# Kernel tuning notes

Hardware: AMD Instinct MI355X
Metric: run time of the kernel (lower is better)

Reference implementation:

```python
import jax, jax.numpy as jnp
import numpy as np

B, S, E, H = 4, 2048, 1024, 16
D = E // H  # head_dim = 64


def setup_inputs() -> dict:
    key0 = jax.random.key(0)
    ks = jax.random.split(key0, 11)
    sc = 1.0 / np.sqrt(E)
    return {
        "query": jax.random.normal(ks[0], (B, S, E), jnp.float32),
        "key": jax.random.normal(ks[1], (B, S, E), jnp.float32),
        "value": jax.random.normal(ks[2], (B, S, E), jnp.float32),
        "Wq": jax.random.normal(ks[3], (E, E), jnp.float32) * sc,
        "bq": jax.random.normal(ks[4], (E,), jnp.float32) * sc,
        "Wk": jax.random.normal(ks[5], (E, E), jnp.float32) * sc,
        "bk": jax.random.normal(ks[6], (E,), jnp.float32) * sc,
        "Wv": jax.random.normal(ks[7], (E, E), jnp.float32) * sc,
        "bv": jax.random.normal(ks[8], (E,), jnp.float32) * sc,
        "Wo": jax.random.normal(ks[9], (E, E), jnp.float32) * sc,
        "bo": jax.random.normal(ks[10], (E,), jnp.float32) * sc,
    }


def reference(query, key, value, Wq, bq, Wk, bk, Wv, bv, Wo, bo):
    b, s, e = query.shape
    q = query @ Wq + bq
    k = key @ Wk + bk
    v = value @ Wv + bv
    # [b, s, E] -> [b, H, s, D]
    qh = q.reshape(b, s, H, D).transpose(0, 2, 1, 3)
    kh = k.reshape(b, s, H, D).transpose(0, 2, 1, 3)
    vh = v.reshape(b, s, H, D).transpose(0, 2, 1, 3)
    energy = jnp.einsum('nhql,nhkl->nhqk', qh, kh)  # [b, H, s, s]
    scale = jnp.asarray(1.0 / np.sqrt(D), energy.dtype)
    attention = jax.nn.softmax(energy * scale, axis=-1)
    # NOTE: faithful to the source einsum 'nhqk,nhvl->nhql' (k and v both contracted)
    out = jnp.einsum('nhqk,nhvl->nhql', attention, vh)  # [b, H, s, D]
    out = out.transpose(0, 2, 1, 3).reshape(b, s, e)
    return out @ Wo + bo
```

## Files before the change

kernel.cpp:

```cpp
#include <hip/hip_runtime.h>
#include <hip/hip_bf16.h>

#define B_ 4
#define S_ 2048
#define E_ 1024

#define ES 16
#define SC 4
#define EPS (E_ / ES)
#define SPC (S_ / SC)
#define NPART (ES * SC)

#define RPB 8

__global__ __launch_bounds__(1024) void k_front(const float* __restrict__ value,
                                                const float* __restrict__ Wv,
                                                const float* __restrict__ bo,
                                                float* __restrict__ tpart,
                                                float* __restrict__ o) {
    const int es = blockIdx.x, sc = blockIdx.y, b = blockIdx.z;
    const int t = threadIdx.x;
    __shared__ float4 red[64][16];
    __shared__ float4 red2[4][16];
    __shared__ float vb[EPS];

    {
        const int c4 = t & 15, rg = t >> 4;
        const float* base = value + ((size_t)b * S_ + (size_t)sc * SPC) * E_
                            + es * EPS + c4 * 4;
        float4 acc = make_float4(0.f, 0.f, 0.f, 0.f);
#pragma unroll
        for (int r = 0; r < 8; ++r) {
            float4 v = *reinterpret_cast<const float4*>(base + (size_t)(rg + r * 64) * E_);
            acc.x += v.x; acc.y += v.y; acc.z += v.z; acc.w += v.w;
        }
        red[rg][c4] = acc;
    }
    __syncthreads();
    if (t < 64) {
        const int c = t & 15, q = t >> 4;
        float4 s = make_float4(0.f, 0.f, 0.f, 0.f);
#pragma unroll
        for (int k = 0; k < 16; ++k) {
            float4 v = red[q * 16 + k][c];
            s.x += v.x; s.y += v.y; s.z += v.z; s.w += v.w;
        }
        red2[q][c] = s;
    }
    __syncthreads();
    if (t < 16) {
        float4 s0 = red2[0][t], s1 = red2[1][t], s2 = red2[2][t], s3 = red2[3][t];
        float4 s = make_float4(s0.x + s1.x + s2.x + s3.x,
                               s0.y + s1.y + s2.y + s3.y,
                               s0.z + s1.z + s2.z + s3.z,
                               s0.w + s1.w + s2.w + s3.w);
        reinterpret_cast<float4*>(vb)[t] = s;
    }
    __syncthreads();

    {
        const float* wv = Wv + (size_t)(es * EPS) * E_ + t;
        float a = 0.f;
#pragma unroll 8
        for (int k = 0; k < EPS; ++k)
            a = fmaf(vb[k], wv[(size_t)k * E_], a);
        tpart[((size_t)(es * SC + sc) * B_ + b) * E_ + t] = a;
    }

    if (es == 0 && sc == 0 && t < 256) {
        reinterpret_cast<float4*>(o + (size_t)b * E_)[t] =
            reinterpret_cast<const float4*>(bo)[t];
    }
}

__global__ __launch_bounds__(256) void k_mid(const float* __restrict__ tpart,
                                             const float* __restrict__ bv,
                                             const float* __restrict__ Wo,
                                             float* __restrict__ o) {
    const int jb = blockIdx.x, b = blockIdx.y;
    const int t = threadIdx.x;
    __shared__ float red[16][16];
    __shared__ float tj[16];

    {
        const int jl = t & 15, pg = t >> 4;
        float s = 0.f;
#pragma unroll
        for (int q = 0; q < 4; ++q) {
            const int p = pg + q * 16;
            s += tpart[((size_t)p * B_ + b) * E_ + jb * 16 + jl];
        }
        red[pg][jl] = s;
    }
    __syncthreads();
    if (t < 16) {
        float v = (float)S_ * bv[jb * 16 + t];
#pragma unroll
        for (int g = 0; g < 16; ++g) v += red[g][t];
        tj[t] = v;
    }
    __syncthreads();

    float oacc[4] = {0.f, 0.f, 0.f, 0.f};
#pragma unroll
    for (int jj = 0; jj < 16; ++jj) {
        const float* wo = Wo + (size_t)(jb * 16 + jj) * E_;
        const float tv = tj[jj];
#pragma unroll
        for (int k2 = 0; k2 < 4; ++k2)
            oacc[k2] = fmaf(tv, wo[k2 * 256 + t], oacc[k2]);
    }
#pragma unroll
    for (int k2 = 0; k2 < 4; ++k2)
        atomicAdd(&o[(size_t)b * E_ + k2 * 256 + t], oacc[k2]);
}

__global__ __launch_bounds__(256) void k_bcast(const float* __restrict__ o,
                                               float* __restrict__ out) {
    const int sb = blockIdx.x, b = blockIdx.y;
    const int t = threadIdx.x;
    float4 ov = reinterpret_cast<const float4*>(o + (size_t)b * E_)[t];
    float4* dst = reinterpret_cast<float4*>(
        out + ((size_t)b * S_ + (size_t)sb * RPB) * E_);
#pragma unroll
    for (int r = 0; r < RPB; ++r)
        dst[r * (E_ / 4) + t] = ov;
}

extern "C" void kernel_launch(void* const* d_in, const int* in_sizes, int n_in,
                              void* d_out, int out_size, void* d_ws, size_t ws_size,
                              hipStream_t stream) {
    const float* value = (const float*)d_in[2];
    const float* Wv    = (const float*)d_in[7];
    const float* bv    = (const float*)d_in[8];
    const float* Wo    = (const float*)d_in[9];
    const float* bo    = (const float*)d_in[10];
    float* out = (float*)d_out;

    float* tpart = (float*)d_ws;
    float* o     = tpart + (size_t)NPART * B_ * E_;

    k_front<<<dim3(ES, SC, B_),    1024, 0, stream>>>(value, Wv, bo, tpart, o);
    k_mid  <<<dim3(NPART, B_),     256,  0, stream>>>(tpart, bv, Wo, o);
    k_bcast<<<dim3(S_ / RPB, B_),  256,  0, stream>>>(o, out);
}
```

Measured before the change: 26.64 us.

## Fuse Wo GEMV and broadcast into a single back kernel, drop atomics

```diff
diff --git a/kernel.cpp b/kernel.cpp
--- a/kernel.cpp
+++ b/kernel.cpp
@@ -11,13 +11,14 @@
 #define SPC (S_ / SC)
 #define NPART (ES * SC)
 
-#define RPB 8
+#define ISL 8
+#define ICW 128
+#define SB 8
+#define RPB2 (S_ / SB)
 
 __global__ __launch_bounds__(1024) void k_front(const float* __restrict__ value,
                                                 const float* __restrict__ Wv,
-                                                const float* __restrict__ bo,
-                                                float* __restrict__ tpart,
-                                                float* __restrict__ o) {
+                                                float* __restrict__ tpart) {
     const int es = blockIdx.x, sc = blockIdx.y, b = blockIdx.z;
     const int t = threadIdx.x;
     __shared__ float4 red[64][16];
@@ -66,65 +67,57 @@
             a = fmaf(vb[k], wv[(size_t)k * E_], a);
         tpart[((size_t)(es * SC + sc) * B_ + b) * E_ + t] = a;
     }
-
-    if (es == 0 && sc == 0 && t < 256) {
-        reinterpret_cast<float4*>(o + (size_t)b * E_)[t] =
-            reinterpret_cast<const float4*>(bo)[t];
-    }
 }
 
-__global__ __launch_bounds__(256) void k_mid(const float* __restrict__ tpart,
-                                             const float* __restrict__ bv,
-                                             const float* __restrict__ Wo,
-                                             float* __restrict__ o) {
-    const int jb = blockIdx.x, b = blockIdx.y;
+__global__ __launch_bounds__(1024) void k_back(const float* __restrict__ tpart,
+                                               const float* __restrict__ bv,
+                                               const float* __restrict__ Wo,
+                                               const float* __restrict__ bo,
+                                               float* __restrict__ out) {
+    const int isl = blockIdx.x, sb = blockIdx.y, b = blockIdx.z;
     const int t = threadIdx.x;
-    __shared__ float red[16][16];
-    __shared__ float tj[16];
+    __shared__ float t_lds[E_];
+    __shared__ float red[8][ICW];
+    __shared__ float o_sl[ICW];
 
     {
-        const int jl = t & 15, pg = t >> 4;
-        float s = 0.f;
-#pragma unroll
-        for (int q = 0; q < 4; ++q) {
-            const int p = pg + q * 16;
-            s += tpart[((size_t)p * B_ + b) * E_ + jb * 16 + jl];
-        }
-        red[pg][jl] = s;
-    }
-    __syncthreads();
-    if (t < 16) {
-        float v = (float)S_ * bv[jb * 16 + t];
-#pragma unroll
-        for (int g = 0; g < 16; ++g) v += red[g][t];
-        tj[t] = v;
+        float s = (float)S_ * bv[t];
+        const float* tp = tpart + (size_t)b * E_ + t;
+#pragma unroll 8
+        for (int p = 0; p < NPART; ++p)
+            s += tp[(size_t)p * (B_ * E_)];
+        t_lds[t] = s;
     }
     __syncthreads();
 
-    float oacc[4] = {0.f, 0.f, 0.f, 0.f};
+    {
+        const int g = t >> 7, cl = t & 127;
+        const float* wo = Wo + (size_t)(g * 128) * E_ + isl * ICW + cl;
+        float acc = 0.f;
+#pragma unroll 8
+        for (int jj = 0; jj < 128; ++jj)
+            acc = fmaf(t_lds[g * 128 + jj], wo[(size_t)jj * E_], acc);
+        red[g][cl] = acc;
+    }
+    __syncthreads();
+    if (t < ICW) {
+        float v = bo[isl * ICW + t];
 #pragma unroll
-    for (int jj = 0; jj < 16; ++jj) {
-        const float* wo = Wo + (size_t)(jb * 16 + jj) * E_;
-        const float tv = tj[jj];
+        for (int g = 0; g < 8; ++g) v += red[g][t];
+        o_sl[t] = v;
+    }
+    __syncthreads();
+
+    {
+        const int c4 = t & 31, rg = t >> 5;
+        const float4 ov = reinterpret_cast<const float4*>(o_sl)[c4];
+        float* base = out + ((size_t)b * S_ + (size_t)sb * RPB2) * E_ + isl * ICW;
 #pragma unroll
-        for (int k2 = 0; k2 < 4; ++k2)
-            oacc[k2] = fmaf(tv, wo[k2 * 256 + t], oacc[k2]);
+        for (int k = 0; k < RPB2 / 32; ++k) {
+            const int row = rg + k * 32;
+            reinterpret_cast<float4*>(base + (size_t)row * E_)[c4] = ov;
+        }
     }
-#pragma unroll
-    for (int k2 = 0; k2 < 4; ++k2)
-        atomicAdd(&o[(size_t)b * E_ + k2 * 256 + t], oacc[k2]);
-}
-
-__global__ __launch_bounds__(256) void k_bcast(const float* __restrict__ o,
-                                               float* __restrict__ out) {
-    const int sb = blockIdx.x, b = blockIdx.y;
-    const int t = threadIdx.x;
-    float4 ov = reinterpret_cast<const float4*>(o + (size_t)b * E_)[t];
-    float4* dst = reinterpret_cast<float4*>(
-        out + ((size_t)b * S_ + (size_t)sb * RPB) * E_);
-#pragma unroll
-    for (int r = 0; r < RPB; ++r)
-        dst[r * (E_ / 4) + t] = ov;
 }
 
 extern "C" void kernel_launch(void* const* d_in, const int* in_sizes, int n_in,
@@ -138,9 +131,7 @@
     float* out = (float*)d_out;
 
     float* tpart = (float*)d_ws;
-    float* o     = tpart + (size_t)NPART * B_ * E_;
 
-    k_front<<<dim3(ES, SC, B_),    1024, 0, stream>>>(value, Wv, bo, tpart, o);
-    k_mid  <<<dim3(NPART, B_),     256,  0, stream>>>(tpart, bv, Wo, o);
-    k_bcast<<<dim3(S_ / RPB, B_),  256,  0, stream>>>(o, out);
+    k_front<<<dim3(ES, SC, B_),  1024, 0, stream>>>(value, Wv, tpart);
+    k_back <<<dim3(ISL, SB, B_), 1024, 0, stream>>>(tpart, bv, Wo, bo, out);
 }
```

Measured after the change: 33.35 us. 25.2% more time.

## Merge mid and broadcast kernels with device-side flag sync and retile front pass

Applied to the files above, without the earlier changes.

```diff
diff --git a/kernel.cpp b/kernel.cpp
--- a/kernel.cpp
+++ b/kernel.cpp
@@ -5,27 +5,30 @@
 #define S_ 2048
 #define E_ 1024
 
-#define ES 16
+#define ES 32
 #define SC 4
-#define EPS (E_ / ES)
-#define SPC (S_ / SC)
+#define EPS 32
+#define SPC 512
 #define NPART (ES * SC)
 
+#define MIDB 256
+#define BCB  1024
 #define RPB 8
 
-__global__ __launch_bounds__(1024) void k_front(const float* __restrict__ value,
-                                                const float* __restrict__ Wv,
-                                                const float* __restrict__ bo,
-                                                float* __restrict__ tpart,
-                                                float* __restrict__ o) {
+__device__ float g_o[B_][E_];
+__device__ int   g_prog[B_];
+__device__ int   g_rdr[B_];
+
+__global__ __launch_bounds__(512) void k_front(const float* __restrict__ value,
+                                               const float* __restrict__ Wv,
+                                               float* __restrict__ tpart) {
     const int es = blockIdx.x, sc = blockIdx.y, b = blockIdx.z;
     const int t = threadIdx.x;
-    __shared__ float4 red[64][16];
-    __shared__ float4 red2[4][16];
+    __shared__ float4 red[64][8];
     __shared__ float vb[EPS];
 
     {
-        const int c4 = t & 15, rg = t >> 4;
+        const int c4 = t & 7, rg = t >> 3;
         const float* base = value + ((size_t)b * S_ + (size_t)sc * SPC) * E_
                             + es * EPS + c4 * 4;
         float4 acc = make_float4(0.f, 0.f, 0.f, 0.f);
@@ -37,94 +40,124 @@
         red[rg][c4] = acc;
     }
     __syncthreads();
-    if (t < 64) {
-        const int c = t & 15, q = t >> 4;
+    if (t < 8) {
         float4 s = make_float4(0.f, 0.f, 0.f, 0.f);
-#pragma unroll
-        for (int k = 0; k < 16; ++k) {
-            float4 v = red[q * 16 + k][c];
+        for (int g = 0; g < 64; ++g) {
+            float4 v = red[g][t];
             s.x += v.x; s.y += v.y; s.z += v.z; s.w += v.w;
         }
-        red2[q][c] = s;
-    }
-    __syncthreads();
-    if (t < 16) {
-        float4 s0 = red2[0][t], s1 = red2[1][t], s2 = red2[2][t], s3 = red2[3][t];
-        float4 s = make_float4(s0.x + s1.x + s2.x + s3.x,
-                               s0.y + s1.y + s2.y + s3.y,
-                               s0.z + s1.z + s2.z + s3.z,
-                               s0.w + s1.w + s2.w + s3.w);
         reinterpret_cast<float4*>(vb)[t] = s;
     }
     __syncthreads();
 
     {
-        const float* wv = Wv + (size_t)(es * EPS) * E_ + t;
-        float a = 0.f;
-#pragma unroll 8
-        for (int k = 0; k < EPS; ++k)
-            a = fmaf(vb[k], wv[(size_t)k * E_], a);
-        tpart[((size_t)(es * SC + sc) * B_ + b) * E_ + t] = a;
-    }
-
-    if (es == 0 && sc == 0 && t < 256) {
-        reinterpret_cast<float4*>(o + (size_t)b * E_)[t] =
-            reinterpret_cast<const float4*>(bo)[t];
+        const float* wv = Wv + (size_t)(es * EPS) * E_;
+        float a0 = 0.f, a1 = 0.f;
+#pragma unroll
+        for (int k = 0; k < EPS; ++k) {
+            const float vk = vb[k];
+            a0 = fmaf(vk, wv[(size_t)k * E_ + t], a0);
+            a1 = fmaf(vk, wv[(size_t)k * E_ + t + 512], a1);
+        }
+        const int p = es * SC + sc;
+        float* dst = tpart + ((size_t)p * B_ + b) * E_;
+        dst[t] = a0;
+        dst[t + 512] = a1;
     }
 }
 
-__global__ __launch_bounds__(256) void k_mid(const float* __restrict__ tpart,
-                                             const float* __restrict__ bv,
-                                             const float* __restrict__ Wo,
-                                             float* __restrict__ o) {
-    const int jb = blockIdx.x, b = blockIdx.y;
+__global__ __launch_bounds__(256) void k_back(const float* __restrict__ tpart,
+                                              const float* __restrict__ bv,
+                                              const float* __restrict__ Wo,
+                                              const float* __restrict__ bo,
+                                              float* __restrict__ out) {
+    const int bid = blockIdx.x;
     const int t = threadIdx.x;
-    __shared__ float red[16][16];
-    __shared__ float tj[16];
 
-    {
-        const int jl = t & 15, pg = t >> 4;
-        float s = 0.f;
+    if (bid < MIDB) {
+        const int jb = bid & 63, b = bid >> 6;
+        __shared__ float red[16][16];
+        __shared__ float tj[16];
+
+        {
+            const int jl = t & 15, pg = t >> 4;
+            float s = 0.f;
 #pragma unroll
-        for (int q = 0; q < 4; ++q) {
-            const int p = pg + q * 16;
-            s += tpart[((size_t)p * B_ + b) * E_ + jb * 16 + jl];
+            for (int q = 0; q < 8; ++q)
+                s += tpart[((size_t)(pg + q * 16) * B_ + b) * E_ + jb * 16 + jl];
+            red[pg][jl] = s;
         }
-        red[pg][jl] = s;
-    }
-    __syncthreads();
-    if (t < 16) {
-        float v = (float)S_ * bv[jb * 16 + t];
+        __syncthreads();
+        if (t < 16) {
+            float v = (float)S_ * bv[jb * 16 + t];
 #pragma unroll
-        for (int g = 0; g < 16; ++g) v += red[g][t];
-        tj[t] = v;
-    }
-    __syncthreads();
+            for (int g = 0; g < 16; ++g) v += red[g][t];
+            tj[t] = v;
+        }
+        __syncthreads();
 
-    float oacc[4] = {0.f, 0.f, 0.f, 0.f};
+        float oacc[4] = {0.f, 0.f, 0.f, 0.f};
 #pragma unroll
-    for (int jj = 0; jj < 16; ++jj) {
-        const float* wo = Wo + (size_t)(jb * 16 + jj) * E_;
-        const float tv = tj[jj];
+        for (int jj = 0; jj < 16; ++jj) {
+            const float* wo = Wo + (size_t)(jb * 16 + jj) * E_;
+            const float tv = tj[jj];
+#pragma unroll
+            for (int k2 = 0; k2 < 4; ++k2)
+                oacc[k2] = fmaf(tv, wo[k2 * 256 + t], oacc[k2]);
+        }
 #pragma unroll
         for (int k2 = 0; k2 < 4; ++k2)
-            oacc[k2] = fmaf(tv, wo[k2 * 256 + t], oacc[k2]);
+            atomicAdd(&g_o[b][k2 * 256 + t], oacc[k2]);
+
+        __threadfence();
+        __syncthreads();
+        if (t == 0) atomicAdd(&g_prog[b], 1);
+    } else {
+        const int id = bid - MIDB;
+        const int sb = id & 255, b = id >> 8;
+        __shared__ int lastflag;
+
+        if (t == 0) {
+            while (__hip_atomic_load(&g_prog[b], __ATOMIC_RELAXED,
+                                     __HIP_MEMORY_SCOPE_AGENT) < 64)
+                __builtin_amdgcn_s_sleep(16);
+        }
+        __syncthreads();
+
+        float o0 = __hip_atomic_load(&g_o[b][t * 4 + 0], __ATOMIC_RELAXED, __HIP_MEMORY_SCOPE_AGENT);
+        float o1 = __hip_atomic_load(&g_o[b][t * 4 + 1], __ATOMIC_RELAXED, __HIP_MEMORY_SCOPE_AGENT);
+        float o2 = __hip_atomic_load(&g_o[b][t * 4 + 2], __ATOMIC_RELAXED, __HIP_MEMORY_SCOPE_AGENT);
+        float o3 = __hip_atomic_load(&g_o[b][t * 4 + 3], __ATOMIC_RELAXED, __HIP_MEMORY_SCOPE_AGENT);
+        float4 bb = reinterpret_cast<const float4*>(bo)[t];
+        float4 ov = make_float4(o0 + bb.x, o1 + bb.y, o2 + bb.z, o3 + bb.w);
+
+        float4* dst = reinterpret_cast<float4*>(
+            out + ((size_t)b * S_ + (size_t)sb * RPB) * E_);
+#pragma unroll
+        for (int r = 0; r < RPB; ++r)
+            dst[r * (E_ / 4) + t] = ov;
+
+        __syncthreads();
+        if (t == 0) {
+            int old = __hip_atomic_fetch_add(&g_rdr[b], 1, __ATOMIC_ACQ_REL,
+                                             __HIP_MEMORY_SCOPE_AGENT);
+            lastflag = (old == 255);
+        }
+        __syncthreads();
+        if (lastflag) {
+            for (int i = t; i < E_; i += 256)
+                __hip_atomic_store(&g_o[b][i], 0.f, __ATOMIC_RELAXED,
+                                   __HIP_MEMORY_SCOPE_AGENT);
+            __threadfence();
+            __syncthreads();
+            if (t == 0) {
+                __hip_atomic_store(&g_rdr[b], 0, __ATOMIC_RELAXED,
+                                   __HIP_MEMORY_SCOPE_AGENT);
+                __hip_atomic_store(&g_prog[b], 0, __ATOMIC_RELAXED,
+                                   __HIP_MEMORY_SCOPE_AGENT);
+            }
+        }
     }
-#pragma unroll
-    for (int k2 = 0; k2 < 4; ++k2)
-        atomicAdd(&o[(size_t)b * E_ + k2 * 256 + t], oacc[k2]);
-}
-
-__global__ __launch_bounds__(256) void k_bcast(const float* __restrict__ o,
-                                               float* __restrict__ out) {
-    const int sb = blockIdx.x, b = blockIdx.y;
-    const int t = threadIdx.x;
-    float4 ov = reinterpret_cast<const float4*>(o + (size_t)b * E_)[t];
-    float4* dst = reinterpret_cast<float4*>(
-        out + ((size_t)b * S_ + (size_t)sb * RPB) * E_);
-#pragma unroll
-    for (int r = 0; r < RPB; ++r)
-        dst[r * (E_ / 4) + t] = ov;
 }
 
 extern "C" void kernel_launch(void* const* d_in, const int* in_sizes, int n_in,
@@ -138,9 +171,7 @@
     float* out = (float*)d_out;
 
     float* tpart = (float*)d_ws;
-    float* o     = tpart + (size_t)NPART * B_ * E_;
 
-    k_front<<<dim3(ES, SC, B_),    1024, 0, stream>>>(value, Wv, bo, tpart, o);
-    k_mid  <<<dim3(NPART, B_),     256,  0, stream>>>(tpart, bv, Wo, o);
-    k_bcast<<<dim3(S_ / RPB, B_),  256,  0, stream>>>(o, out);
+    k_front<<<dim3(ES, SC, B_), 512, 0, stream>>>(value, Wv, tpart);
+    k_back <<<dim3(MIDB + BCB), 256, 0, stream>>>(tpart, bv, Wo, bo, out);
 }
```

After: 89.10 us. 234% more time.
